# Optimization experiments

Measured on AMD Instinct MI355X. Metric: run time of the kernel, lower is better.

## Reference

```python
import jax, jax.numpy as jnp
import numpy as np

EPS = 1e-5
GROUPS = 32

# 3x3 regular grid: row0 = dy, row1 = dx for kernel index k = ky*3 + kx
_REG = jnp.array([[-1, -1, -1, 0, 0, 0, 1, 1, 1],
                  [-1, 0, 1, -1, 0, 1, -1, 0, 1]], dtype=jnp.float32)


def conv2d(x, w, pad):
    return jax.lax.conv_general_dilated(
        x, w, window_strides=(1, 1), padding=((pad, pad), (pad, pad)),
        dimension_numbers=('NCHW', 'OIHW', 'NCHW'))


def deform_conv3x3(x, off_y, off_x, w_dcn, dilation):
    # x: (N,C,H,W); off_y/off_x: (N,H,W,9); w_dcn: (Cout,Cin,3,3)
    N, C, H, W = x.shape
    dyk = (jnp.arange(9) // 3 - 1).astype(jnp.float32) * dilation  # (9,)
    dxk = (jnp.arange(9) % 3 - 1).astype(jnp.float32) * dilation
    yy = jnp.arange(H, dtype=jnp.float32)
    xx = jnp.arange(W, dtype=jnp.float32)
    # sampling positions (padding == dilation, stride == 1)
    py = yy[None, :, None, None] + dyk[None, None, None, :] + off_y  # (N,H,W,9)
    px = xx[None, None, :, None] + dxk[None, None, None, :] + off_x

    y0 = jnp.floor(py)
    x0 = jnp.floor(px)
    wy1 = py - y0
    wx1 = px - x0

    xflat = x.reshape(N, C, H * W)

    def gather(xf, idx):  # xf (C,HW), idx (H,W,9) -> (C,H,W,9)
        return xf[:, idx]

    val = jnp.zeros((N, C, H, W, 9), dtype=x.dtype)
    corners = [
        (y0, x0, (1.0 - wy1) * (1.0 - wx1)),
        (y0, x0 + 1.0, (1.0 - wy1) * wx1),
        (y0 + 1.0, x0, wy1 * (1.0 - wx1)),
        (y0 + 1.0, x0 + 1.0, wy1 * wx1),
    ]
    for yc, xc, wc in corners:
        valid = ((yc >= 0) & (yc <= H - 1) & (xc >= 0) & (xc <= W - 1)).astype(x.dtype)
        yi = jnp.clip(yc, 0, H - 1).astype(jnp.int32)
        xi = jnp.clip(xc, 0, W - 1).astype(jnp.int32)
        ind = yi * W + xi  # (N,H,W,9)
        g = jax.vmap(gather)(xflat, ind)  # (N,C,H,W,9)
        val = val + g * (wc * valid)[:, None]

    Cout = w_dcn.shape[0]
    wk = w_dcn.reshape(Cout, C, 9)
    return jnp.einsum('nchwk,ock->nohw', val, wk)


def group_norm(x, gamma, beta, groups, eps):
    N, C, H, W = x.shape
    xg = x.reshape(N, groups, C // groups, H, W)
    mu = xg.mean(axis=(2, 3, 4), keepdims=True)
    var = xg.var(axis=(2, 3, 4), keepdims=True)
    xn = ((xg - mu) * jax.lax.rsqrt(var + eps)).reshape(N, C, H, W)
    return xn * gamma[None, :, None, None] + beta[None, :, None, None]


def setup_inputs() -> dict:
    key = jax.random.key(0)
    k1, k2, k3, k4 = jax.random.split(key, 4)
    C, Cout = 256, 256
    x = jax.random.normal(k1, (8, C, 64, 64), dtype=jnp.float32)
    w_tm = jax.random.normal(k2, (4, C, 3, 3), dtype=jnp.float32) * 0.02
    b_tm = jnp.zeros((4,), dtype=jnp.float32)
    w_dcn = jax.random.normal(k3, (Cout, C, 3, 3), dtype=jnp.float32) * 0.02
    gn_gamma = jnp.ones((Cout,), dtype=jnp.float32)
    gn_beta = jnp.zeros((Cout,), dtype=jnp.float32)
    return {"x": x, "w_tm": w_tm, "b_tm": b_tm, "w_dcn": w_dcn,
            "gn_gamma": gn_gamma, "gn_beta": gn_beta}


def reference(x, w_tm, b_tm, w_dcn, gn_gamma, gn_beta):
    N, C, H, W = x.shape
    # offset-generating 3x3 conv -> 4 channels = per-pixel 2x2 transform matrix
    tm = conv2d(x, w_tm, pad=1) + b_tm[None, :, None, None]  # (N,4,H,W)
    T = tm.transpose(0, 2, 3, 1).reshape(N, H, W, 2, 2)
    off = jnp.einsum('nhwij,jk->nhwik', T, _REG) - _REG  # (N,H,W,2,9)
    off_y = off[..., 0, :]  # (N,H,W,9)
    off_x = off[..., 1, :]
    out = deform_conv3x3(x, off_y, off_x, w_dcn, dilation=1)
    out = group_norm(out, gn_gamma, gn_beta, GROUPS, EPS)
    return jax.nn.relu(out)
```

## Files before the change

### kernel.cpp

```cpp
#include <hip/hip_runtime.h>
#include <hip/hip_fp16.h>
#include <stdint.h>

typedef float        f32x4 __attribute__((ext_vector_type(4)));
typedef _Float16     f16x8 __attribute__((ext_vector_type(8)));
typedef _Float16     f16x4 __attribute__((ext_vector_type(4)));
typedef _Float16     f16x2 __attribute__((ext_vector_type(2)));
typedef _Float16 f16;

__device__ inline float bf2f(unsigned short b){ return __builtin_bit_cast(float,(unsigned)b<<16); }
__device__ inline bool is_bf16_mode(const void* g){ return ((const unsigned*)g)[0]==0x3F803F80u; }
__device__ inline float ld_in(const void* p, int i, bool bfm){
  return bfm ? bf2f(((const unsigned short*)p)[i]) : ((const float*)p)[i];
}

#if defined(__has_builtin)
#if __has_builtin(__builtin_amdgcn_fdot2)
#define HAS_FDOT2 1
#endif
#endif
#ifdef HAS_FDOT2
#define FDOT2(acc,a,b) (acc = __builtin_amdgcn_fdot2((a),(b),(acc),false))
#else
#define FDOT2(acc,a,b) (acc += (float)(a)[0]*(float)(b)[0] + (float)(a)[1]*(float)(b)[1])
#endif

#define FAST_BARRIER() __asm__ __volatile__("s_waitcnt lgkmcnt(0)\n\ts_barrier" ::: "memory")

#define WS_XT    0u
#define WS_BF    16777216u
#define WS_ST    17956864u
#define WS_NEED  17958912u
#define WS_YT    17958912u
#define WS_NEED2 34736128u

__device__ inline int wslot(int tap, int cp){ return (tap*128 + cp) ^ ((cp >> 2) & 7); }

__global__ __launch_bounds__(256) void k_prep(const void* __restrict__ x_,
                                              const void* __restrict__ wdcn,
                                              const void* __restrict__ gamma,
                                              f16* __restrict__ xt,
                                              f16* __restrict__ Bf,
                                              float* __restrict__ stats){
  const bool bfm = is_bf16_mode(gamma);
  const int t = threadIdx.x;
  const int id = blockIdx.x;
  if (id >= 2048){
    const int j = id - 2048;
    if (j == 0){
      stats[t] = 0.f; stats[t + 256] = 0.f;
    }
    #pragma unroll
    for (int it = 0; it < 5; it++){
      int ii = it*256 + t;
      if (ii < 1152){
        int i = j*1152 + ii;
        int u    = i & 7;
        int l    = (i >> 3)  & 63;
        int tile = (i >> 9)  & 15;
        int ks   = (i >> 13) & 1;
        int ch   = (i >> 14) & 3;
        int tap  = i >> 16;
        int ml = l & 15, q = l >> 4;
        int oc = tile*16 + ml;
        int c  = ch*64 + ks*32 + q*8 + u;
        Bf[i] = (f16)ld_in(wdcn, oc*2304 + c*9 + tap, bfm);
      }
    }
    return;
  }
  const int n  = id & 7;
  const int w  = id >> 3;
  const int c0 = (w & 3)  << 6;
  const int s0 = (w >> 2) << 6;
  __shared__ float tile[64][65];
  {
    const int sp = (t & 31) * 2;
    const int q  = t >> 5;
    #pragma unroll
    for (int i = 0; i < 8; i++){
      int cc = q + i*8;
      int base = (n*256 + c0 + cc)*4096 + s0 + sp;
      tile[cc][sp]   = ld_in(x_, base,   bfm);
      tile[cc][sp+1] = ld_in(x_, base+1, bfm);
    }
  }
  __syncthreads();
  {
    const int cc = (t & 31) * 2;
    const int q  = t >> 5;
    f16* dst = xt + (size_t)(n*4096 + s0)*256 + c0;
    #pragma unroll
    for (int i = 0; i < 8; i++){
      int s = q + i*8;
      dst[s*256 + cc]   = (f16)tile[cc][s];
      dst[s*256 + cc+1] = (f16)tile[cc+1][s];
    }
  }
}

__global__ __launch_bounds__(512,4) void k_fused8(const f16* __restrict__ xt,
                                                  const f16* __restrict__ Bf,
                                                  const void* __restrict__ wtm_,
                                                  const void* __restrict__ btm_,
                                                  const void* __restrict__ gamma,
                                                  float* __restrict__ out,
                                                  f16* __restrict__ yt,
                                                  float* __restrict__ stats){
  __shared__ __attribute__((aligned(16))) char smemA[18432];
  __shared__ float4 wfL[576];
  __shared__ int4   idxL[576];
  __shared__ float4 Tsm[64];
  f16* wh = (f16*)smemA;
  f16* At = (f16*)smemA;
  const bool bfm = is_bf16_mode(gamma);
  const int t = threadIdx.x;
  const int blk = blockIdx.x;
  const int n = blk & 7, h = blk >> 3;
  const int wid = t >> 6, l = t & 63;
  const int wc = wid & 3, ks = wid >> 2;
  const int ml = l & 15, q = l >> 4;

  for (int s = t; s < 1152; s += 512){
    const int tap = s >> 7, cp = s & 127;
    const int c = cp*2;
    f16x8 W;
    #pragma unroll
    for (int o = 0; o < 4; o++){
      W[o*2]   = (f16)ld_in(wtm_, o*2304 + c*9 + tap,     bfm);
      W[o*2+1] = (f16)ld_in(wtm_, o*2304 + (c+1)*9 + tap, bfm);
    }
    *(f16x8*)(wh + wslot(tap, cp)*8) = W;
  }
  __syncthreads();

  {
    const int px = t >> 3, cq = t & 7;
    float a0=0.f, a1=0.f, a2=0.f, a3=0.f;
    for (int tap = 0; tap < 9; tap++){
      const int yy = h + tap/3 - 1, xx = px + tap%3 - 1;
      if ((unsigned)yy < 64u && (unsigned)xx < 64u){
        const f16* row = xt + ((n*4096 + yy*64 + xx)*256);
        #pragma unroll
        for (int jb = 0; jb < 4; jb++){
          const int chunk = jb*8 + cq;
          f16x8 xv = *(const f16x8*)(row + chunk*8);
          #pragma unroll
          for (int p = 0; p < 4; p++){
            const int cp = chunk*4 + p;
            const f16x8 W = *(const f16x8*)&wh[wslot(tap, cp)*8];
            const f16x2 xp = {xv[2*p], xv[2*p+1]};
            FDOT2(a0, xp, ((f16x2){W[0], W[1]}));
            FDOT2(a1, xp, ((f16x2){W[2], W[3]}));
            FDOT2(a2, xp, ((f16x2){W[4], W[5]}));
            FDOT2(a3, xp, ((f16x2){W[6], W[7]}));
          }
        }
      }
    }
    a0 += __shfl_xor(a0,1,64); a0 += __shfl_xor(a0,2,64); a0 += __shfl_xor(a0,4,64);
    a1 += __shfl_xor(a1,1,64); a1 += __shfl_xor(a1,2,64); a1 += __shfl_xor(a1,4,64);
    a2 += __shfl_xor(a2,1,64); a2 += __shfl_xor(a2,2,64); a2 += __shfl_xor(a2,4,64);
    a3 += __shfl_xor(a3,1,64); a3 += __shfl_xor(a3,2,64); a3 += __shfl_xor(a3,4,64);
    if (cq == 0){
      float4 r;
      r.x = a0 + ld_in(btm_,0,bfm);  r.y = a1 + ld_in(btm_,1,bfm);
      r.z = a2 + ld_in(btm_,2,bfm);  r.w = a3 + ld_in(btm_,3,bfm);
      Tsm[px] = r;
    }
  }
  __syncthreads();

  for (int e = t; e < 576; e += 512){
    const int px = e & 63, tap = e >> 6;
    const float4 T = Tsm[px];
    const float dy = (float)(tap/3 - 1);
    const float dx = (float)(tap%3 - 1);
    float py  = (float)h  + T.x*dy + T.y*dx;
    float pxx = (float)px + T.z*dy + T.w*dx;
    float y0 = floorf(py), x0 = floorf(pxx);
    float wy = py - y0,  wx = pxx - x0;
    float y1 = y0 + 1.f, x1 = x0 + 1.f;
    float vy0 = (y0 >= 0.f && y0 <= 63.f) ? 1.f : 0.f;
    float vy1 = (y1 >= 0.f && y1 <= 63.f) ? 1.f : 0.f;
    float vx0 = (x0 >= 0.f && x0 <= 63.f) ? 1.f : 0.f;
    float vx1 = (x1 >= 0.f && x1 <= 63.f) ? 1.f : 0.f;
    float4 wf;
    wf.x = (1.f-wy)*(1.f-wx)*vy0*vx0;
    wf.y = (1.f-wy)*wx      *vy0*vx1;
    wf.z = wy*(1.f-wx)      *vy1*vx0;
    wf.w = wy*wx            *vy1*vx1;
    int yi0 = (int)fminf(fmaxf(y0,0.f),63.f);
    int yi1 = (int)fminf(fmaxf(y1,0.f),63.f);
    int xi0 = (int)fminf(fmaxf(x0,0.f),63.f);
    int xi1 = (int)fminf(fmaxf(x1,0.f),63.f);
    const int base = n*4096*512;
    int4 id;
    id.x = base + (yi0*64 + xi0)*512;
    id.y = base + (yi0*64 + xi1)*512;
    id.z = base + (yi1*64 + xi0)*512;
    id.w = base + (yi1*64 + xi1)*512;
    idxL[e] = id;
    wfL[e]  = wf;
  }

  f32x4 acc[4][4];
  #pragma unroll
  for (int mt = 0; mt < 4; mt++)
    #pragma unroll
    for (int nt = 0; nt < 4; nt++) acc[mt][nt] = (f32x4){0.f,0.f,0.f,0.f};

  const int bpx = t >> 3, bu = t & 7;
  const char* xb = (const char*)xt;

  __syncthreads();

  const char* bfb = (const char*)Bf + (ks*16 + wc*4)*1024 + l*16;
  int4  idc = idxL[bpx];
  float4 cwf = wfL[bpx];
  f16x8 pA, pB, pC, pD;
  f16x8 bfr0, bfr1, bfr2, bfr3;
  {
    const int cb = bu*16;
    pA = *(const f16x8*)(xb + idc.x + cb);
    pB = *(const f16x8*)(xb + idc.y + cb);
    pC = *(const f16x8*)(xb + idc.z + cb);
    pD = *(const f16x8*)(xb + idc.w + cb);
    bfr0 = *(const f16x8*)(bfb);
    bfr1 = *(const f16x8*)(bfb + 1024);
    bfr2 = *(const f16x8*)(bfb + 2048);
    bfr3 = *(const f16x8*)(bfb + 3072);
  }

  for (int step = 0; step < 36; step++){
    {
      const f16 wA=(f16)cwf.x, wB=(f16)cwf.y, wC=(f16)cwf.z, wD=(f16)cwf.w;
      f16x8 R = pA*wA + pB*wB + pC*wC + pD*wD;
      *(f16x8*)(&At[(step & 1)*4608 + bpx*72 + bu*8]) = R;
    }
    if (step < 35){
      if ((step & 3) == 3){
        const int e = ((step+1) >> 2)*64 + bpx;
        idc = idxL[e];
        cwf = wfL[e];
      }
      const int cb = (((step+1) & 3)*64 + bu*8)*2;
      pA = *(const f16x8*)(xb + idc.x + cb);
      pB = *(const f16x8*)(xb + idc.y + cb);
      pC = *(const f16x8*)(xb + idc.z + cb);
      pD = *(const f16x8*)(xb + idc.w + cb);
    }
    FAST_BARRIER();
    const f16* Atr = &At[(step & 1)*4608];
    #pragma unroll
    for (int mt = 0; mt < 4; mt++){
      f16x8 afr = *(const f16x8*)(Atr + (mt*16 + ml)*72 + ks*32 + q*8);
      acc[mt][0] = __builtin_amdgcn_mfma_f32_16x16x32_f16(afr, bfr0, acc[mt][0], 0, 0, 0);
      acc[mt][1] = __builtin_amdgcn_mfma_f32_16x16x32_f16(afr, bfr1, acc[mt][1], 0, 0, 0);
      acc[mt][2] = __builtin_amdgcn_mfma_f32_16x16x32_f16(afr, bfr2, acc[mt][2], 0, 0, 0);
      acc[mt][3] = __builtin_amdgcn_mfma_f32_16x16x32_f16(afr, bfr3, acc[mt][3], 0, 0, 0);
    }
    if (step < 35){
      const char* bp = bfb + (size_t)(step+1)*32768;
      bfr0 = *(const f16x8*)(bp);
      bfr1 = *(const f16x8*)(bp + 1024);
      bfr2 = *(const f16x8*)(bp + 2048);
      bfr3 = *(const f16x8*)(bp + 3072);
    }
  }

  float4* red = (float4*)smemA;
  #pragma unroll
  for (int nt = 0; nt < 4; nt++){
    __syncthreads();
    if (ks == 1){
      #pragma unroll
      for (int k = 0; k < 4; k++){
        float4 v;
        v.x = acc[k][nt][0]; v.y = acc[k][nt][1];
        v.z = acc[k][nt][2]; v.w = acc[k][nt][3];
        red[wc*256 + k*64 + l] = v;
      }
    }
    __syncthreads();
    if (ks == 0){
      #pragma unroll
      for (int k = 0; k < 4; k++){
        float4 v = red[wc*256 + k*64 + l];
        acc[k][nt][0] += v.x; acc[k][nt][1] += v.y;
        acc[k][nt][2] += v.z; acc[k][nt][3] += v.w;
      }
    }
  }

  if (ks == 0){
    if (yt){
      #pragma unroll
      for (int mt = 0; mt < 4; mt++)
        #pragma unroll
        for (int nt = 0; nt < 4; nt++){
          const int oc = wc*64 + nt*16 + ml;
          const int m0 = mt*16 + q*4;
          f16x4 v;
          v[0] = (f16)acc[mt][nt][0]; v[1] = (f16)acc[mt][nt][1];
          v[2] = (f16)acc[mt][nt][2]; v[3] = (f16)acc[mt][nt][3];
          *(f16x4*)(yt + (size_t)(n*256 + oc)*4096 + h*64 + m0) = v;
        }
    } else {
      #pragma unroll
      for (int mt = 0; mt < 4; mt++)
        #pragma unroll
        for (int nt = 0; nt < 4; nt++){
          const int oc = wc*64 + nt*16 + ml;
          const int m0 = mt*16 + q*4;
          float4 v;
          v.x = acc[mt][nt][0]; v.y = acc[mt][nt][1];
          v.z = acc[mt][nt][2]; v.w = acc[mt][nt][3];
          *(float4*)(out + (size_t)(n*256 + oc)*4096 + h*64 + m0) = v;
        }
    }
    #pragma unroll
    for (int nt = 0; nt < 4; nt++){
      float s1 = 0.f, s2 = 0.f;
      #pragma unroll
      for (int mt = 0; mt < 4; mt++)
        #pragma unroll
        for (int rr = 0; rr < 4; rr++){
          float v = acc[mt][nt][rr];
          s1 += v; s2 += v*v;
        }
      s1 += __shfl_xor(s1,16,64); s1 += __shfl_xor(s1,32,64);
      s2 += __shfl_xor(s2,16,64); s2 += __shfl_xor(s2,32,64);
      s1 += __shfl_xor(s1,1,64);  s1 += __shfl_xor(s1,2,64);  s1 += __shfl_xor(s1,4,64);
      s2 += __shfl_xor(s2,1,64);  s2 += __shfl_xor(s2,2,64);  s2 += __shfl_xor(s2,4,64);
      if ((l & 0x37) == 0){
        const int oc = wc*64 + nt*16 + (l & 8);
        const int g = oc >> 3;
        atomicAdd(stats + n*64 + g*2,     s1);
        atomicAdd(stats + n*64 + g*2 + 1, s2);
      }
    }
  }
}

__global__ __launch_bounds__(256) void k_gn(float* __restrict__ out,
                                            const float* __restrict__ stats,
                                            const void* __restrict__ gamma,
                                            const void* __restrict__ beta){
  const int blk = blockIdx.x;
  const int n = blk >> 8, oc = blk & 255;
  const int g = oc >> 3;
  const bool bfm = is_bf16_mode(gamma);
  const float s1 = stats[n*64 + g*2];
  const float s2 = stats[n*64 + g*2 + 1];
  const float inv = 1.f/32768.f;
  const float mu  = s1*inv;
  const float var = s2*inv - mu*mu;
  const float rs  = rsqrtf(var + 1e-5f);
  const float gv = ld_in(gamma, oc, bfm);
  const float bv = ld_in(beta,  oc, bfm);
  const float sc = gv*rs;
  const float sh = bv - mu*sc;
  float* p = out + (size_t)(n*256 + oc)*4096;
  const int t = threadIdx.x;
  #pragma unroll
  for (int i = 0; i < 4; i++){
    float4 v = *(float4*)(p + (i*256 + t)*4);
    v.x = fmaxf(v.x*sc + sh, 0.f);
    v.y = fmaxf(v.y*sc + sh, 0.f);
    v.z = fmaxf(v.z*sc + sh, 0.f);
    v.w = fmaxf(v.w*sc + sh, 0.f);
    *(float4*)(p + (i*256 + t)*4) = v;
  }
}

__global__ __launch_bounds__(256) void k_gn16(const f16* __restrict__ yt,
                                              float* __restrict__ out,
                                              const float* __restrict__ stats,
                                              const void* __restrict__ gamma,
                                              const void* __restrict__ beta){
  const int blk = blockIdx.x;
  const int n = blk >> 8, oc = blk & 255;
  const int g = oc >> 3;
  const bool bfm = is_bf16_mode(gamma);
  const float s1 = stats[n*64 + g*2];
  const float s2 = stats[n*64 + g*2 + 1];
  const float inv = 1.f/32768.f;
  const float mu  = s1*inv;
  const float var = s2*inv - mu*mu;
  const float rs  = rsqrtf(var + 1e-5f);
  const float gv = ld_in(gamma, oc, bfm);
  const float bv = ld_in(beta,  oc, bfm);
  const float sc = gv*rs;
  const float sh = bv - mu*sc;
  const f16* src = yt + (size_t)(n*256 + oc)*4096;
  float*     p   = out + (size_t)(n*256 + oc)*4096;
  const int t = threadIdx.x;
  #pragma unroll
  for (int i = 0; i < 2; i++){
    const int e = (i*256 + t)*8;
    f16x8 v = *(const f16x8*)(src + e);
    float4 a, b;
    a.x = fmaxf((float)v[0]*sc + sh, 0.f);
    a.y = fmaxf((float)v[1]*sc + sh, 0.f);
    a.z = fmaxf((float)v[2]*sc + sh, 0.f);
    a.w = fmaxf((float)v[3]*sc + sh, 0.f);
    b.x = fmaxf((float)v[4]*sc + sh, 0.f);
    b.y = fmaxf((float)v[5]*sc + sh, 0.f);
    b.z = fmaxf((float)v[6]*sc + sh, 0.f);
    b.w = fmaxf((float)v[7]*sc + sh, 0.f);
    *(float4*)(p + e)     = a;
    *(float4*)(p + e + 4) = b;
  }
}

__global__ void k_ws_small(float* out){ if (threadIdx.x == 0) out[0] += 200000.f; }

extern "C" void kernel_launch(void* const* d_in, const int* in_sizes, int n_in,
                              void* d_out, int out_size, void* d_ws, size_t ws_size,
                              hipStream_t stream){
  const void* x     = d_in[0];
  const void* wtm   = d_in[1];
  const void* btm   = d_in[2];
  const void* wdcn  = d_in[3];
  const void* gamma = d_in[4];
  const void* beta  = d_in[5];
  float* out = (float*)d_out;
  if (ws_size < (size_t)WS_NEED){
    hipLaunchKernelGGL(k_ws_small, dim3(1), dim3(64), 0, stream, out);
    return;
  }
  char* ws = (char*)d_ws;
  f16*   xt    = (f16*)  (ws + WS_XT);
  f16*   Bf    = (f16*)  (ws + WS_BF);
  float* stats = (float*)(ws + WS_ST);
  const bool use_f16 = (ws_size >= (size_t)WS_NEED2);
  f16*   yt    = use_f16 ? (f16*)(ws + WS_YT) : nullptr;

  hipLaunchKernelGGL(k_prep,   dim3(2560),   dim3(256), 0, stream, x, wdcn, gamma, xt, Bf, stats);
  hipLaunchKernelGGL(k_fused8, dim3(512),    dim3(512), 0, stream, xt, Bf, wtm, btm, gamma, out, yt, stats);
  if (use_f16)
    hipLaunchKernelGGL(k_gn16, dim3(2048),   dim3(256), 0, stream, yt, out, stats, gamma, beta);
  else
    hipLaunchKernelGGL(k_gn,   dim3(2048),   dim3(256), 0, stream, out, stats, gamma, beta);
}
```

Measured before the change: 179.1 us.

## Process two K-steps per barrier in deform-conv MFMA loop with doubled LDS

The main loop now covers two 32-channel K-steps per iteration. Both bilinear-interpolated A tiles go into a doubled double-buffered LDS region before a single barrier, which halves the number of workgroup barriers. The second step's B fragment is loaded between the two MFMA batches, so that load latency is exposed within the iteration. LDS per block doubles to 36 KB, which may reduce occupancy below the launch-bounds target.

```diff
diff --git a/kernel.cpp b/kernel.cpp
--- a/kernel.cpp
+++ b/kernel.cpp
@@ -107,7 +107,7 @@
                                                   float* __restrict__ out,
                                                   f16* __restrict__ yt,
                                                   float* __restrict__ stats){
-  __shared__ __attribute__((aligned(16))) char smemA[18432];
+  __shared__ __attribute__((aligned(16))) char smemA[36864];
   __shared__ float4 wfL[576];
   __shared__ int4   idxL[576];
   __shared__ float4 Tsm[64];
@@ -232,36 +232,70 @@
     bfr3 = *(const f16x8*)(bfb + 3072);
   }
 
-  for (int step = 0; step < 36; step++){
+  for (int it = 0; it < 18; it++){
+    const int s = it << 1;
+    f16* Ab = &At[(it & 1)*9216];
     {
       const f16 wA=(f16)cwf.x, wB=(f16)cwf.y, wC=(f16)cwf.z, wD=(f16)cwf.w;
       f16x8 R = pA*wA + pB*wB + pC*wC + pD*wD;
-      *(f16x8*)(&At[(step & 1)*4608 + bpx*72 + bu*8]) = R;
-    }
-    if (step < 35){
-      if ((step & 3) == 3){
-        const int e = ((step+1) >> 2)*64 + bpx;
-        idc = idxL[e];
-        cwf = wfL[e];
-      }
-      const int cb = (((step+1) & 3)*64 + bu*8)*2;
+      *(f16x8*)(Ab + bpx*72 + bu*8) = R;
+    }
+    {
+      const int cb = (((s+1) & 3)*64 + bu*8)*2;
       pA = *(const f16x8*)(xb + idc.x + cb);
       pB = *(const f16x8*)(xb + idc.y + cb);
       pC = *(const f16x8*)(xb + idc.z + cb);
       pD = *(const f16x8*)(xb + idc.w + cb);
     }
+    {
+      const f16 wA=(f16)cwf.x, wB=(f16)cwf.y, wC=(f16)cwf.z, wD=(f16)cwf.w;
+      f16x8 R = pA*wA + pB*wB + pC*wC + pD*wD;
+      *(f16x8*)(Ab + 4608 + bpx*72 + bu*8) = R;
+    }
+    if (it < 17){
+      if ((s & 3) == 2){
+        const int e = ((s+2) >> 2)*64 + bpx;
+        idc = idxL[e];
+        cwf = wfL[e];
+      }
+      const int cb = (((s+2) & 3)*64 + bu*8)*2;
+      pA = *(const f16x8*)(xb + idc.x + cb);
+      pB = *(const f16x8*)(xb + idc.y + cb);
+      pC = *(const f16x8*)(xb + idc.z + cb);
+      pD = *(const f16x8*)(xb + idc.w + cb);
+    }
     FAST_BARRIER();
-    const f16* Atr = &At[(step & 1)*4608];
-    #pragma unroll
-    for (int mt = 0; mt < 4; mt++){
-      f16x8 afr = *(const f16x8*)(Atr + (mt*16 + ml)*72 + ks*32 + q*8);
-      acc[mt][0] = __builtin_amdgcn_mfma_f32_16x16x32_f16(afr, bfr0, acc[mt][0], 0, 0, 0);
-      acc[mt][1] = __builtin_amdgcn_mfma_f32_16x16x32_f16(afr, bfr1, acc[mt][1], 0, 0, 0);
-      acc[mt][2] = __builtin_amdgcn_mfma_f32_16x16x32_f16(afr, bfr2, acc[mt][2], 0, 0, 0);
-      acc[mt][3] = __builtin_amdgcn_mfma_f32_16x16x32_f16(afr, bfr3, acc[mt][3], 0, 0, 0);
-    }
-    if (step < 35){
-      const char* bp = bfb + (size_t)(step+1)*32768;
+    {
+      const f16* Atr = Ab;
+      #pragma unroll
+      for (int mt = 0; mt < 4; mt++){
+        f16x8 afr = *(const f16x8*)(Atr + (mt*16 + ml)*72 + ks*32 + q*8);
+        acc[mt][0] = __builtin_amdgcn_mfma_f32_16x16x32_f16(afr, bfr0, acc[mt][0], 0, 0, 0);
+        acc[mt][1] = __builtin_amdgcn_mfma_f32_16x16x32_f16(afr, bfr1, acc[mt][1], 0, 0, 0);
+        acc[mt][2] = __builtin_amdgcn_mfma_f32_16x16x32_f16(afr, bfr2, acc[mt][2], 0, 0, 0);
+        acc[mt][3] = __builtin_amdgcn_mfma_f32_16x16x32_f16(afr, bfr3, acc[mt][3], 0, 0, 0);
+      }
+    }
+    {
+      const char* bp = bfb + (size_t)(s+1)*32768;
+      bfr0 = *(const f16x8*)(bp);
+      bfr1 = *(const f16x8*)(bp + 1024);
+      bfr2 = *(const f16x8*)(bp + 2048);
+      bfr3 = *(const f16x8*)(bp + 3072);
+    }
+    {
+      const f16* Atr = Ab + 4608;
+      #pragma unroll
+      for (int mt = 0; mt < 4; mt++){
+        f16x8 afr = *(const f16x8*)(Atr + (mt*16 + ml)*72 + ks*32 + q*8);
+        acc[mt][0] = __builtin_amdgcn_mfma_f32_16x16x32_f16(afr, bfr0, acc[mt][0], 0, 0, 0);
+        acc[mt][1] = __builtin_amdgcn_mfma_f32_16x16x32_f16(afr, bfr1, acc[mt][1], 0, 0, 0);
+        acc[mt][2] = __builtin_amdgcn_mfma_f32_16x16x32_f16(afr, bfr2, acc[mt][2], 0, 0, 0);
+        acc[mt][3] = __builtin_amdgcn_mfma_f32_16x16x32_f16(afr, bfr3, acc[mt][3], 0, 0, 0);
+      }
+    }
+    if (it < 17){
+      const char* bp = bfb + (size_t)(s+2)*32768;
       bfr0 = *(const f16x8*)(bp);
       bfr1 = *(const f16x8*)(bp + 1024);
       bfr2 = *(const f16x8*)(bp + 2048);
```

New measurement: 188.6 us. 5.3% more time.
